# Performance work log

Measured on AMD Instinct MI355X. Metric: run time of the kernel, lower is better.

## Reference

```python
import jax, jax.numpy as jnp
import numpy as np

N_NODES = 10000
N_EDGES = 320000
IN_F = 256
OUT_F = 256
SLOPE = 0.2


def setup_inputs() -> dict:
    key = jax.random.key(0)
    ks = jax.random.split(key, 8)
    features = jax.random.normal(ks[0], (N_NODES, IN_F), dtype=jnp.float32)
    edge_u = jax.random.randint(ks[1], (N_EDGES,), 0, N_NODES)
    edge_v = jax.random.randint(ks[2], (N_EDGES,), 0, N_NODES)
    s = 1.0 / np.sqrt(IN_F)
    W = jax.random.uniform(ks[3], (IN_F, OUT_F), minval=-s, maxval=s, dtype=jnp.float32)
    b_lin = jax.random.uniform(ks[4], (OUT_F,), minval=-s, maxval=s, dtype=jnp.float32)
    sa = 1.0 / np.sqrt(2 * OUT_F)
    # attention Linear(2*OUT_F, 1) split into source/dest halves
    Wa_src = jax.random.uniform(ks[5], (OUT_F,), minval=-sa, maxval=sa, dtype=jnp.float32)
    Wa_dst = jax.random.uniform(ks[6], (OUT_F,), minval=-sa, maxval=sa, dtype=jnp.float32)
    b_att = jax.random.uniform(ks[7], (), minval=-sa, maxval=sa, dtype=jnp.float32)
    return {"features": features, "edge_u": edge_u, "edge_v": edge_v,
            "W": W, "b_lin": b_lin, "Wa_src": Wa_src, "Wa_dst": Wa_dst, "b_att": b_att}


def reference(features, edge_u, edge_v, W, b_lin, Wa_src, Wa_dst, b_att):
    # Wh = linear(inputs): [N, OUT_F]
    Wh = features @ W + b_lin
    # per-edge attention logit: attention(cat(Wh[u], Wh[v])) -> scalar, fully vectorized
    e = Wh[edge_u] @ Wa_src + Wh[edge_v] @ Wa_dst + b_att  # [E]
    n = features.shape[0]
    # dense coeffs matrix with symmetric scatter, exactly as the torch loop builds it
    coeffs = jnp.zeros((n, n), dtype=features.dtype)
    coeffs = coeffs.at[edge_u, edge_v].set(e)
    coeffs = coeffs.at[edge_v, edge_u].set(e)
    # leaky_relu then row softmax over ALL nodes (non-edges contribute exp(0)=1, as in the original)
    alpha = jax.nn.softmax(jax.nn.leaky_relu(coeffs, negative_slope=SLOPE), axis=1)
    return jax.nn.elu(alpha @ Wh)
```

## Files before the change

kernel.cpp:

```cpp
#include <hip/hip_runtime.h>
#include <math.h>

#define N_NODES 10000
#define N_EDGES 320000
#define IN_F 256
#define OUT_F 256
#define SLOPE 0.2f
#define CAP 128

using f32x4 = __attribute__((ext_vector_type(4))) float;
using s16x8 = __attribute__((ext_vector_type(8))) short;
using u16x8 = __attribute__((ext_vector_type(8))) unsigned short;

__device__ __forceinline__ unsigned short f2bf_rtn(float x) {
    unsigned int u = __float_as_uint(x);
    u = (u + 0x7FFFu + ((u >> 16) & 1u)) >> 16;
    return (unsigned short)u;
}
__device__ __forceinline__ float bf_lo(unsigned int u) { return __uint_as_float(u << 16); }
__device__ __forceinline__ float bf_hi(unsigned int u) { return __uint_as_float(u & 0xFFFF0000u); }

__global__ __launch_bounds__(256) void wconv_kernel(const float* __restrict__ W,
                                                    unsigned short* __restrict__ WbfT) {
    __shared__ unsigned short t[64][72];
    const int tid = threadIdx.x;
    const int k0 = (blockIdx.x >> 2) * 64, n0 = (blockIdx.x & 3) * 64;
#pragma unroll
    for (int i = 0; i < 16; ++i) {
        const int idx = i * 256 + tid;
        const int kk = idx >> 6, nn = idx & 63;
        t[nn][kk] = f2bf_rtn(W[(size_t)(k0 + kk) * 256 + n0 + nn]);
    }
    __syncthreads();
#pragma unroll
    for (int i = 0; i < 4; ++i) {
        const int q = i * 256 + tid;
        const int nn = q >> 4, ch = q & 15;
        *(ushort4*)(WbfT + (size_t)(n0 + nn) * 256 + k0 + ch * 4) =
            *(const ushort4*)&t[nn][ch * 4];
    }
}

__global__ __launch_bounds__(64, 1) void wh_kernel(
    const float* __restrict__ feat, const unsigned short* __restrict__ WbfT,
    const float* __restrict__ b, const float* __restrict__ Was,
    const float* __restrict__ Wad, unsigned short* __restrict__ WhB,
    float* __restrict__ ds, float* __restrict__ dd, float* __restrict__ S)
{
    __shared__ unsigned short lt[16][264];
    const int l = threadIdx.x;
    const int c = l & 15, h = l >> 4;
    const int rbase = blockIdx.x * 16;

    float wasv[16], wadv[16];
    f32x4 acc[16];
#pragma unroll
    for (int nt = 0; nt < 16; ++nt) {
        wasv[nt] = Was[nt * 16 + c];
        wadv[nt] = Wad[nt * 16 + c];
        const float bv = b[nt * 16 + c];
        acc[nt] = (f32x4){bv, bv, bv, bv};
    }

    const float* arow = feat + (size_t)(rbase + c) * IN_F + h * 8;
    const unsigned short* bbase = WbfT + (size_t)c * 256 + h * 8;
#pragma unroll
    for (int kt = 0; kt < 8; ++kt) {
        const float4 f0 = *(const float4*)(arow + kt * 32);
        const float4 f1 = *(const float4*)(arow + kt * 32 + 4);
        s16x8 a;
        a[0] = (short)f2bf_rtn(f0.x); a[1] = (short)f2bf_rtn(f0.y);
        a[2] = (short)f2bf_rtn(f0.z); a[3] = (short)f2bf_rtn(f0.w);
        a[4] = (short)f2bf_rtn(f1.x); a[5] = (short)f2bf_rtn(f1.y);
        a[6] = (short)f2bf_rtn(f1.z); a[7] = (short)f2bf_rtn(f1.w);
        s16x8 bb[16];
#pragma unroll
        for (int nt = 0; nt < 16; ++nt)
            bb[nt] = *(const s16x8*)(bbase + (size_t)nt * 16 * 256 + kt * 32);
#pragma unroll
        for (int nt = 0; nt < 16; ++nt)
            acc[nt] = __builtin_amdgcn_mfma_f32_16x16x32_bf16(a, bb[nt], acc[nt], 0, 0, 0);
    }

    float pds[4] = {0.f, 0.f, 0.f, 0.f}, pdd[4] = {0.f, 0.f, 0.f, 0.f};
#pragma unroll
    for (int nt = 0; nt < 16; ++nt)
#pragma unroll
        for (int r = 0; r < 4; ++r) {
            pds[r] = fmaf(acc[nt][r], wasv[nt], pds[r]);
            pdd[r] = fmaf(acc[nt][r], wadv[nt], pdd[r]);
        }
#pragma unroll
    for (int r = 0; r < 4; ++r) {
#pragma unroll
        for (int m = 1; m < 16; m <<= 1) {
            pds[r] += __shfl_xor(pds[r], m);
            pdd[r] += __shfl_xor(pdd[r], m);
        }
    }
    if (c == 0) {
#pragma unroll
        for (int r = 0; r < 4; ++r) {
            ds[rbase + h * 4 + r] = pds[r];
            dd[rbase + h * 4 + r] = pdd[r];
        }
    }

#pragma unroll
    for (int nt = 0; nt < 16; ++nt) {
        float v = (acc[nt][0] + acc[nt][1]) + (acc[nt][2] + acc[nt][3]);
        v += __shfl_xor(v, 16);
        v += __shfl_xor(v, 32);
        if (h == 0) atomicAdd(&S[nt * 16 + c], v);
    }

#pragma unroll
    for (int nt = 0; nt < 16; ++nt)
#pragma unroll
        for (int r = 0; r < 4; ++r)
            lt[h * 4 + r][nt * 16 + c] = f2bf_rtn(acc[nt][r]);
    __syncthreads();
#pragma unroll
    for (int i = 0; i < 8; ++i) {
        const int g = i * 64 + l;
        const int row = g >> 5, ch = g & 31;
        ((u16x8*)(WhB + (size_t)rbase * 256))[g] = *(const u16x8*)&lt[row][ch * 8];
    }
}

__global__ void scatter_kernel(const int* __restrict__ eu, const int* __restrict__ ev,
                               int* __restrict__ cnt, int* __restrict__ slots) {
    const int i = blockIdx.x * blockDim.x + threadIdx.x;
    if (i >= N_EDGES) return;
    const int u = eu[i], v = ev[i];
    const int p = atomicAdd(&cnt[u], 1);
    if (p < CAP) slots[u * CAP + p] = (v << 1);
    const int q = atomicAdd(&cnt[v], 1);
    if (q < CAP) slots[v * CAP + q] = (u << 1) | 1;
}

__global__ __launch_bounds__(256) void row_kernel(
    const unsigned short* __restrict__ WhB, const float* __restrict__ S,
    const int* __restrict__ cnt, const int* __restrict__ slots,
    const float* __restrict__ gd,
    const float* __restrict__ batt, float* __restrict__ out)
{
    __shared__ __attribute__((aligned(16))) float sw[CAP];
    __shared__ __attribute__((aligned(16))) int   scol[CAP];
    __shared__ __attribute__((aligned(16))) int   sq[CAP + 4];
    __shared__ float comb[3][64][4];
    __shared__ float wspart[4];
    const int r   = blockIdx.x;
    const int tid = threadIdx.x;
    const int w   = tid >> 6;
    const int l   = tid & 63;
    int k = cnt[r];
    if (k > CAP) k = CAP;
    const float ddr = gd[r], dsr = gd[N_NODES + r], bA = batt[0];
    if (tid < CAP) {
        if (tid < k) {
            const int s = slots[(size_t)r * CAP + tid];
            const int c = s >> 1, ph = s & 1;
            scol[tid] = c;
            sq[tid]   = (c << 8) | (ph << 7) | (127 - tid);
            const float e = (gd[ph * N_NODES + c] + (ph ? ddr : dsr)) + bA;
            const float lr = e >= 0.f ? e : SLOPE * e;
            sw[tid] = __expf(lr) - 1.f;
        } else { scol[tid] = 0; sq[tid] = 1 << 30; sw[tid] = 0.f; }
    } else if (tid < CAP + 4) {
        sq[tid] = 1 << 30;
    }
    __syncthreads();
    if (tid < k) {
        const int qj = sq[tid], cj = qj >> 8;
        const int4* q4 = (const int4*)sq;
        const int kk4 = (k + 3) >> 2;
        bool dup = false;
        for (int t = 0; t < kk4; ++t) {
            const int4 qq = q4[t];
            dup = dup | ((qq.x >> 8) == cj && qq.x > qj)
                      | ((qq.y >> 8) == cj && qq.y > qj)
                      | ((qq.z >> 8) == cj && qq.z > qj)
                      | ((qq.w >> 8) == cj && qq.w > qj);
        }
        if (dup) sw[tid] = 0.f;
    }
    __syncthreads();

    const int k32 = (k + 31) & ~31;
    const int kq  = k32 >> 2;
    const int j0  = w * kq;
    const uint2* wp = (const uint2*)WhB + l;
    float a0 = 0.f, a1 = 0.f, a2 = 0.f, a3 = 0.f;
    float b0 = 0.f, b1 = 0.f, b2 = 0.f, b3 = 0.f;
    float s = 0.f;
    for (int j = j0; j < j0 + kq; j += 8) {
        const float4 wa = *(const float4*)&sw[j];
        const float4 wb = *(const float4*)&sw[j + 4];
        const int4   ca = *(const int4*)&scol[j];
        const int4   cb = *(const int4*)&scol[j + 4];
        const uint2 u0 = wp[(size_t)ca.x << 6];
        const uint2 u1 = wp[(size_t)ca.y << 6];
        const uint2 u2 = wp[(size_t)ca.z << 6];
        const uint2 u3 = wp[(size_t)ca.w << 6];
        const uint2 u4 = wp[(size_t)cb.x << 6];
        const uint2 u5 = wp[(size_t)cb.y << 6];
        const uint2 u6 = wp[(size_t)cb.z << 6];
        const uint2 u7 = wp[(size_t)cb.w << 6];
        a0 = fmaf(wa.x, bf_lo(u0.x), a0); a1 = fmaf(wa.x, bf_hi(u0.x), a1);
        a2 = fmaf(wa.x, bf_lo(u0.y), a2); a3 = fmaf(wa.x, bf_hi(u0.y), a3);
        b0 = fmaf(wa.y, bf_lo(u1.x), b0); b1 = fmaf(wa.y, bf_hi(u1.x), b1);
        b2 = fmaf(wa.y, bf_lo(u1.y), b2); b3 = fmaf(wa.y, bf_hi(u1.y), b3);
        a0 = fmaf(wa.z, bf_lo(u2.x), a0); a1 = fmaf(wa.z, bf_hi(u2.x), a1);
        a2 = fmaf(wa.z, bf_lo(u2.y), a2); a3 = fmaf(wa.z, bf_hi(u2.y), a3);
        b0 = fmaf(wa.w, bf_lo(u3.x), b0); b1 = fmaf(wa.w, bf_hi(u3.x), b1);
        b2 = fmaf(wa.w, bf_lo(u3.y), b2); b3 = fmaf(wa.w, bf_hi(u3.y), b3);
        a0 = fmaf(wb.x, bf_lo(u4.x), a0); a1 = fmaf(wb.x, bf_hi(u4.x), a1);
        a2 = fmaf(wb.x, bf_lo(u4.y), a2); a3 = fmaf(wb.x, bf_hi(u4.y), a3);
        b0 = fmaf(wb.y, bf_lo(u5.x), b0); b1 = fmaf(wb.y, bf_hi(u5.x), b1);
        b2 = fmaf(wb.y, bf_lo(u5.y), b2); b3 = fmaf(wb.y, bf_hi(u5.y), b3);
        a0 = fmaf(wb.z, bf_lo(u6.x), a0); a1 = fmaf(wb.z, bf_hi(u6.x), a1);
        a2 = fmaf(wb.z, bf_lo(u6.y), a2); a3 = fmaf(wb.z, bf_hi(u6.y), a3);
        b0 = fmaf(wb.w, bf_lo(u7.x), b0); b1 = fmaf(wb.w, bf_hi(u7.x), b1);
        b2 = fmaf(wb.w, bf_lo(u7.y), b2); b3 = fmaf(wb.w, bf_hi(u7.y), b3);
        s += ((wa.x + wa.y) + (wa.z + wa.w)) + ((wb.x + wb.y) + (wb.z + wb.w));
    }
    const float p0 = a0 + b0, p1 = a1 + b1, p2 = a2 + b2, p3 = a3 + b3;
    if (w) {
        float4 p; p.x = p0; p.y = p1; p.z = p2; p.w = p3;
        *(float4*)comb[w - 1][l] = p;
        if (l == 0) wspart[w] = s;
    } else if (l == 0) wspart[0] = s;
    __syncthreads();
    if (w == 0) {
        const float4 q0 = *(const float4*)comb[0][l];
        const float4 q1 = *(const float4*)comb[1][l];
        const float4 q2 = *(const float4*)comb[2][l];
        const float Z = (float)N_NODES + ((wspart[0] + wspart[1]) + (wspart[2] + wspart[3]));
        const float4 S4 = ((const float4*)S)[l];
        const float y0 = (S4.x + ((p0 + q0.x) + (q1.x + q2.x))) / Z;
        const float y1 = (S4.y + ((p1 + q0.y) + (q1.y + q2.y))) / Z;
        const float y2 = (S4.z + ((p2 + q0.z) + (q1.z + q2.z))) / Z;
        const float y3 = (S4.w + ((p3 + q0.w) + (q1.w + q2.w))) / Z;
        float4 o;
        o.x = y0 > 0.f ? y0 : expm1f(y0);
        o.y = y1 > 0.f ? y1 : expm1f(y1);
        o.z = y2 > 0.f ? y2 : expm1f(y2);
        o.w = y3 > 0.f ? y3 : expm1f(y3);
        ((float4*)(out + (size_t)r * OUT_F))[l] = o;
    }
}

extern "C" void kernel_launch(void* const* d_in, const int* in_sizes, int n_in,
                              void* d_out, int out_size, void* d_ws, size_t ws_size,
                              hipStream_t stream) {
    const float* feat = (const float*)d_in[0];
    const int*   eu   = (const int*)d_in[1];
    const int*   ev   = (const int*)d_in[2];
    const float* W    = (const float*)d_in[3];
    const float* blin = (const float*)d_in[4];
    const float* Was  = (const float*)d_in[5];
    const float* Wad  = (const float*)d_in[6];
    const float* batt = (const float*)d_in[7];
    float* out = (float*)d_out;

    char* p = (char*)d_ws;
    int* slots = (int*)p;                     p += (size_t)N_NODES * CAP * 4;
    unsigned short* WhB = (unsigned short*)p; p += (size_t)N_NODES * OUT_F * 2;
    unsigned short* WbfT = (unsigned short*)p; p += (size_t)IN_F * OUT_F * 2;
    float* S    = (float*)p;                  p += OUT_F * 4;
    int*   cnt  = (int*)p;                    p += N_NODES * 4;
    float* gd   = (float*)p;                  p += 2 * N_NODES * 4;
    float* ddv  = gd;
    float* dsv  = gd + N_NODES;

    hipMemsetAsync(S, 0, OUT_F * sizeof(float) + N_NODES * sizeof(int), stream);

    wconv_kernel  <<<16,                    256, 0, stream>>>(W, WbfT);
    wh_kernel     <<<N_NODES / 16,          64,  0, stream>>>(feat, WbfT, blin, Was, Wad, WhB, dsv, ddv, S);
    scatter_kernel<<<(N_EDGES + 255) / 256, 256, 0, stream>>>(eu, ev, cnt, slots);
    row_kernel    <<<N_NODES,               256, 0, stream>>>(WhB, S, cnt, slots, gd, batt, out);
}
```

Measured before the change: 184.8 us.

## Split Wh GEMM block across eight waves by output columns with shared bf16 features

```diff
diff --git a/kernel.cpp b/kernel.cpp
--- a/kernel.cpp
+++ b/kernel.cpp
@@ -41,55 +41,59 @@
     }
 }
 
-__global__ __launch_bounds__(64, 1) void wh_kernel(
+__global__ __launch_bounds__(512) void wh_kernel(
     const float* __restrict__ feat, const unsigned short* __restrict__ WbfT,
     const float* __restrict__ b, const float* __restrict__ Was,
     const float* __restrict__ Wad, unsigned short* __restrict__ WhB,
     float* __restrict__ ds, float* __restrict__ dd, float* __restrict__ S)
 {
-    __shared__ unsigned short lt[16][264];
-    const int l = threadIdx.x;
+    __shared__ unsigned short sfb[16][264];
+    __shared__ float dsred[8][16];
+    __shared__ float ddred[8][16];
+    const int tid = threadIdx.x;
+    const int l = tid & 63, w = tid >> 6;
     const int c = l & 15, h = l >> 4;
     const int rbase = blockIdx.x * 16;
-
-    float wasv[16], wadv[16];
-    f32x4 acc[16];
-#pragma unroll
-    for (int nt = 0; nt < 16; ++nt) {
-        wasv[nt] = Was[nt * 16 + c];
-        wadv[nt] = Wad[nt * 16 + c];
-        const float bv = b[nt * 16 + c];
+    const int col0 = w * 32;
+
+    {
+        const float4* src = (const float4*)(feat + (size_t)rbase * IN_F);
+        for (int i = tid; i < 1024; i += 512) {
+            const float4 f = src[i];
+            ushort4 pk;
+            pk.x = f2bf_rtn(f.x); pk.y = f2bf_rtn(f.y);
+            pk.z = f2bf_rtn(f.z); pk.w = f2bf_rtn(f.w);
+            *(ushort4*)&sfb[i >> 6][(i & 63) * 4] = pk;
+        }
+    }
+    __syncthreads();
+
+    float wasv[2], wadv[2];
+    f32x4 acc[2];
+#pragma unroll
+    for (int nt = 0; nt < 2; ++nt) {
+        const int gc = col0 + nt * 16 + c;
+        wasv[nt] = Was[gc]; wadv[nt] = Wad[gc];
+        const float bv = b[gc];
         acc[nt] = (f32x4){bv, bv, bv, bv};
     }
 
-    const float* arow = feat + (size_t)(rbase + c) * IN_F + h * 8;
-    const unsigned short* bbase = WbfT + (size_t)c * 256 + h * 8;
+    const unsigned short* bbase = WbfT + (size_t)(col0 + c) * 256 + h * 8;
 #pragma unroll
     for (int kt = 0; kt < 8; ++kt) {
-        const float4 f0 = *(const float4*)(arow + kt * 32);
-        const float4 f1 = *(const float4*)(arow + kt * 32 + 4);
-        s16x8 a;
-        a[0] = (short)f2bf_rtn(f0.x); a[1] = (short)f2bf_rtn(f0.y);
-        a[2] = (short)f2bf_rtn(f0.z); a[3] = (short)f2bf_rtn(f0.w);
-        a[4] = (short)f2bf_rtn(f1.x); a[5] = (short)f2bf_rtn(f1.y);
-        a[6] = (short)f2bf_rtn(f1.z); a[7] = (short)f2bf_rtn(f1.w);
-        s16x8 bb[16];
-#pragma unroll
-        for (int nt = 0; nt < 16; ++nt)
-            bb[nt] = *(const s16x8*)(bbase + (size_t)nt * 16 * 256 + kt * 32);
-#pragma unroll
-        for (int nt = 0; nt < 16; ++nt)
-            acc[nt] = __builtin_amdgcn_mfma_f32_16x16x32_bf16(a, bb[nt], acc[nt], 0, 0, 0);
-    }
-
-    float pds[4] = {0.f, 0.f, 0.f, 0.f}, pdd[4] = {0.f, 0.f, 0.f, 0.f};
-#pragma unroll
-    for (int nt = 0; nt < 16; ++nt)
-#pragma unroll
-        for (int r = 0; r < 4; ++r) {
-            pds[r] = fmaf(acc[nt][r], wasv[nt], pds[r]);
-            pdd[r] = fmaf(acc[nt][r], wadv[nt], pdd[r]);
-        }
+        const s16x8 a  = *(const s16x8*)&sfb[c][kt * 32 + h * 8];
+        const s16x8 b0 = *(const s16x8*)(bbase + kt * 32);
+        const s16x8 b1 = *(const s16x8*)(bbase + 16 * 256 + kt * 32);
+        acc[0] = __builtin_amdgcn_mfma_f32_16x16x32_bf16(a, b0, acc[0], 0, 0, 0);
+        acc[1] = __builtin_amdgcn_mfma_f32_16x16x32_bf16(a, b1, acc[1], 0, 0, 0);
+    }
+
+    float pds[4], pdd[4];
+#pragma unroll
+    for (int r = 0; r < 4; ++r) {
+        pds[r] = acc[0][r] * wasv[0] + acc[1][r] * wasv[1];
+        pdd[r] = acc[0][r] * wadv[0] + acc[1][r] * wadv[1];
+    }
 #pragma unroll
     for (int r = 0; r < 4; ++r) {
 #pragma unroll
@@ -101,30 +105,37 @@
     if (c == 0) {
 #pragma unroll
         for (int r = 0; r < 4; ++r) {
-            ds[rbase + h * 4 + r] = pds[r];
-            dd[rbase + h * 4 + r] = pdd[r];
-        }
-    }
-
-#pragma unroll
-    for (int nt = 0; nt < 16; ++nt) {
+            dsred[w][h * 4 + r] = pds[r];
+            ddred[w][h * 4 + r] = pdd[r];
+        }
+    }
+
+#pragma unroll
+    for (int nt = 0; nt < 2; ++nt) {
         float v = (acc[nt][0] + acc[nt][1]) + (acc[nt][2] + acc[nt][3]);
         v += __shfl_xor(v, 16);
         v += __shfl_xor(v, 32);
-        if (h == 0) atomicAdd(&S[nt * 16 + c], v);
-    }
-
-#pragma unroll
-    for (int nt = 0; nt < 16; ++nt)
+        if (h == 0) atomicAdd(&S[col0 + nt * 16 + c], v);
+    }
+    __syncthreads();
+
+    if (tid < 16) {
+        float s1 = 0.f, s2 = 0.f;
+#pragma unroll
+        for (int ww = 0; ww < 8; ++ww) { s1 += dsred[ww][tid]; s2 += ddred[ww][tid]; }
+        ds[rbase + tid] = s1;
+        dd[rbase + tid] = s2;
+    }
+
+#pragma unroll
+    for (int nt = 0; nt < 2; ++nt)
 #pragma unroll
         for (int r = 0; r < 4; ++r)
-            lt[h * 4 + r][nt * 16 + c] = f2bf_rtn(acc[nt][r]);
-    __syncthreads();
-#pragma unroll
-    for (int i = 0; i < 8; ++i) {
-        const int g = i * 64 + l;
-        const int row = g >> 5, ch = g & 31;
-        ((u16x8*)(WhB + (size_t)rbase * 256))[g] = *(const u16x8*)&lt[row][ch * 8];
+            sfb[h * 4 + r][col0 + nt * 16 + c] = f2bf_rtn(acc[nt][r]);
+    __syncthreads();
+    {
+        const int row = tid >> 5, ch = tid & 31;
+        *(u16x8*)(WhB + (size_t)(rbase + row) * 256 + ch * 8) = *(const u16x8*)&sfb[row][ch * 8];
     }
 }
 
@@ -277,7 +288,7 @@
     hipMemsetAsync(S, 0, OUT_F * sizeof(float) + N_NODES * sizeof(int), stream);
 
     wconv_kernel  <<<16,                    256, 0, stream>>>(W, WbfT);
-    wh_kernel     <<<N_NODES / 16,          64,  0, stream>>>(feat, WbfT, blin, Was, Wad, WhB, dsv, ddv, S);
+    wh_kernel     <<<N_NODES / 16,          512, 0, stream>>>(feat, WbfT, blin, Was, Wad, WhB, dsv, ddv, S);
     scatter_kernel<<<(N_EDGES + 255) / 256, 256, 0, stream>>>(eu, ev, cnt, slots);
     row_kernel    <<<N_NODES,               256, 0, stream>>>(WhB, S, cnt, slots, gd, batt, out);
 }
```

After: 181.1 us. -2.0%, faster.
